# Kernel optimization log

Hardware: AMD Instinct MI355X
Metric: run time of the kernel (lower is better)

The kernel has to match this reference:

```python
import jax, jax.numpy as jnp
import numpy as np

B, SEQ, ST, DIN, DK, DV = 2, 4096, 128, 1024, 64, 64
T = SEQ + 2 * ST  # 4352, divisible by 8 -> no pad branch in original


def _l2norm(t):
    # matches torch F.normalize(p=2, dim=-1, eps=1e-12)
    return t / jnp.maximum(jnp.linalg.norm(t, axis=-1, keepdims=True), 1e-12)


def setup_inputs() -> dict:
    key = jax.random.key(0)
    ks = jax.random.split(key, 9)
    x = jax.random.normal(ks[0], (B, T, DIN), dtype=jnp.float32)
    w = 0.02
    Wq = jax.random.normal(ks[1], (DK, DIN), dtype=jnp.float32) * w
    Wk = jax.random.normal(ks[2], (DK, DIN), dtype=jnp.float32) * w
    Wv = jax.random.normal(ks[3], (DV, DIN), dtype=jnp.float32) * w
    Wq_s = jax.random.normal(ks[4], (DK, DIN), dtype=jnp.float32) * w
    Wk_s = jax.random.normal(ks[5], (DK, DIN), dtype=jnp.float32) * w
    Wv_s = jax.random.normal(ks[6], (DV, DIN), dtype=jnp.float32) * w
    cope_emb = jax.random.normal(ks[7], (DK, T), dtype=jnp.float32)  # (1, dim_key, seq_len+2*state_len) squeezed
    scale = jnp.array([0.125], dtype=jnp.float32)  # learnable scaling_factor param
    return {"x": x, "Wq": Wq, "Wk": Wk, "Wv": Wv, "Wq_s": Wq_s,
            "Wk_s": Wk_s, "Wv_s": Wv_s, "cope_emb": cope_emb, "scale": scale}


def reference(x, Wq, Wk, Wv, Wq_s, Wk_s, Wv_s, cope_emb, scale):
    # extract_state: start-state, sequence, end-state
    xs, xm, xe = x[:, :ST], x[:, ST:ST + SEQ], x[:, ST + SEQ:]
    # project (Linear, no bias) then L2-normalize each token vector
    q = jnp.concatenate([_l2norm(xs @ Wq_s.T), _l2norm(xm @ Wq.T), _l2norm(xe @ Wq_s.T)], axis=1)
    k = jnp.concatenate([_l2norm(xs @ Wk_s.T), _l2norm(xm @ Wk.T), _l2norm(xe @ Wk_s.T)], axis=1)
    v = jnp.concatenate([_l2norm(xs @ Wv_s.T), _l2norm(xm @ Wv.T), _l2norm(xe @ Wv_s.T)], axis=1)

    # q@k^T is used both for CoPE gates and (scaled) attention scores
    logits = jnp.einsum('btd,bsd->bts', q, k)  # (B, T, T)

    # --- CoPE bias ---
    gates = jax.nn.sigmoid(logits)
    pos = jnp.cumsum(gates[:, :, ::-1], axis=-1)[:, :, ::-1]  # flip-cumsum-flip
    pos = jnp.minimum(pos, jnp.float32(T - 1))
    pos_floor = jnp.floor(pos)
    pos_ceil = jnp.ceil(pos)
    w = pos - pos_floor
    logits_int = jnp.einsum('btd,dl->btl', q, cope_emb)  # (B, T, T)
    lc = jnp.take_along_axis(logits_int, pos_ceil.astype(jnp.int32), axis=-1)
    lf = jnp.take_along_axis(logits_int, pos_floor.astype(jnp.int32), axis=-1)
    cope_bias = lc * w + lf * (1.0 - w)

    # --- causal + state-token mask: tril, with end-state rows blocked from start-state cols ---
    i = jnp.arange(T)
    mask = i[:, None] >= i[None, :]
    blocked = (i[:, None] >= SEQ + ST) & (i[None, :] < ST)
    mask = mask & (~blocked)
    attn_bias = jnp.where(mask, 0.0, -jnp.inf)[None, :, :]

    scores = logits * scale[0] + attn_bias + cope_bias
    att = jax.nn.softmax(scores, axis=-1) @ v  # (B, T, DV)
    return att
```

## Files before the change

kernel.cpp:

```cpp
#include <hip/hip_runtime.h>
#include <math.h>

#define B_ 2
#define SEQ_ 4096
#define ST_ 128
#define T_ 4352
#define DIN_ 1024
#define NW 16
#define LMAX 3328
#define LPAD 3336
#define NSLICE 272
#define NROW 8704

typedef _Float16 f16;
typedef __attribute__((ext_vector_type(8))) _Float16 f16x8;
typedef __attribute__((ext_vector_type(4))) float f32x4;

#define OB_WH  0
#define OB_WL  786432
#define OB_QH  1572864
#define OB_QL  2686976
#define OB_KH  3801088
#define OB_KL  4915200
#define OB_VT  6029312
#define OB_CPT 7143424
#define OB_SS  7569408
#define OB_XH  17039360
#define OB_XL  34865152
#define NEED_NEW 52690944ull

#define WT4_OFF 0
#define Q_OFF   393216
#define KT_OFF  950272
#define V_OFF   1507328

__device__ __forceinline__ int wuid() {
  return __builtin_amdgcn_readfirstlane((int)(threadIdx.x >> 6));
}

template<int CTRL, int RM>
__device__ __forceinline__ float dppadd(float x) {
  int y = __builtin_amdgcn_update_dpp(0, __float_as_int(x), CTRL, RM, 0xf, true);
  return x + __int_as_float(y);
}
__device__ __forceinline__ float wave_iscan(float x) {
  x = dppadd<0x111, 0xf>(x);
  x = dppadd<0x112, 0xf>(x);
  x = dppadd<0x114, 0xf>(x);
  x = dppadd<0x118, 0xf>(x);
  x = dppadd<0x142, 0xa>(x);
  x = dppadd<0x143, 0xc>(x);
  return x;
}
__device__ __forceinline__ float p16scan(float x) {
  x = dppadd<0x111, 0xf>(x);
  x = dppadd<0x112, 0xf>(x);
  x = dppadd<0x114, 0xf>(x);
  x = dppadd<0x118, 0xf>(x);
  return x;
}
__device__ __forceinline__ float swz15(float x) {
  return __int_as_float(__builtin_amdgcn_ds_swizzle(__float_as_int(x), 0x1F0));
}

__global__ __launch_bounds__(256) void wsplit_kernel(
    const float* __restrict__ Wq,  const float* __restrict__ Wk,
    const float* __restrict__ Wv,  const float* __restrict__ Wqs,
    const float* __restrict__ Wks, const float* __restrict__ Wvs,
    f16* __restrict__ wh, f16* __restrict__ wl) {
  const int m = blockIdx.y;
  const float* src = (m==0)?Wq:(m==1)?Wqs:(m==2)?Wk:(m==3)?Wks:(m==4)?Wv:Wvs;
  const int g0 = (int)blockIdx.x * 4096 + (int)threadIdx.x * 16;
  const float4* s4 = reinterpret_cast<const float4*>(src + g0);
  float4 v0 = s4[0], v1 = s4[1], v2 = s4[2], v3 = s4[3];
  f16x8 h0, h1, l0, l1;
  h0[0]=(f16)v0.x; h0[1]=(f16)v0.y; h0[2]=(f16)v0.z; h0[3]=(f16)v0.w;
  h0[4]=(f16)v1.x; h0[5]=(f16)v1.y; h0[6]=(f16)v1.z; h0[7]=(f16)v1.w;
  h1[0]=(f16)v2.x; h1[1]=(f16)v2.y; h1[2]=(f16)v2.z; h1[3]=(f16)v2.w;
  h1[4]=(f16)v3.x; h1[5]=(f16)v3.y; h1[6]=(f16)v3.z; h1[7]=(f16)v3.w;
  l0[0]=(f16)(v0.x-(float)h0[0]); l0[1]=(f16)(v0.y-(float)h0[1]);
  l0[2]=(f16)(v0.z-(float)h0[2]); l0[3]=(f16)(v0.w-(float)h0[3]);
  l0[4]=(f16)(v1.x-(float)h0[4]); l0[5]=(f16)(v1.y-(float)h0[5]);
  l0[6]=(f16)(v1.z-(float)h0[6]); l0[7]=(f16)(v1.w-(float)h0[7]);
  l1[0]=(f16)(v2.x-(float)h1[0]); l1[1]=(f16)(v2.y-(float)h1[1]);
  l1[2]=(f16)(v2.z-(float)h1[2]); l1[3]=(f16)(v2.w-(float)h1[3]);
  l1[4]=(f16)(v3.x-(float)h1[4]); l1[5]=(f16)(v3.y-(float)h1[5]);
  l1[6]=(f16)(v3.z-(float)h1[6]); l1[7]=(f16)(v3.w-(float)h1[7]);
  const size_t o = (size_t)m * 65536 + g0;
  *reinterpret_cast<f16x8*>(wh + o) = h0;
  *reinterpret_cast<f16x8*>(wh + o + 8) = h1;
  *reinterpret_cast<f16x8*>(wl + o) = l0;
  *reinterpret_cast<f16x8*>(wl + o + 8) = l1;
}

__global__ __launch_bounds__(256) void xsplit_kernel(
    const float* __restrict__ x, f16* __restrict__ xh, f16* __restrict__ xl) {
  const size_t g0 = ((size_t)blockIdx.x * 256 + threadIdx.x) * 16;
  const float4* s4 = reinterpret_cast<const float4*>(x + g0);
  float4 v0 = s4[0], v1 = s4[1], v2 = s4[2], v3 = s4[3];
  f16x8 h0, h1, l0, l1;
  h0[0]=(f16)v0.x; h0[1]=(f16)v0.y; h0[2]=(f16)v0.z; h0[3]=(f16)v0.w;
  h0[4]=(f16)v1.x; h0[5]=(f16)v1.y; h0[6]=(f16)v1.z; h0[7]=(f16)v1.w;
  h1[0]=(f16)v2.x; h1[1]=(f16)v2.y; h1[2]=(f16)v2.z; h1[3]=(f16)v2.w;
  h1[4]=(f16)v3.x; h1[5]=(f16)v3.y; h1[6]=(f16)v3.z; h1[7]=(f16)v3.w;
  l0[0]=(f16)(v0.x-(float)h0[0]); l0[1]=(f16)(v0.y-(float)h0[1]);
  l0[2]=(f16)(v0.z-(float)h0[2]); l0[3]=(f16)(v0.w-(float)h0[3]);
  l0[4]=(f16)(v1.x-(float)h0[4]); l0[5]=(f16)(v1.y-(float)h0[5]);
  l0[6]=(f16)(v1.z-(float)h0[6]); l0[7]=(f16)(v1.w-(float)h0[7]);
  l1[0]=(f16)(v2.x-(float)h1[0]); l1[1]=(f16)(v2.y-(float)h1[1]);
  l1[2]=(f16)(v2.z-(float)h1[2]); l1[3]=(f16)(v2.w-(float)h1[3]);
  l1[4]=(f16)(v3.x-(float)h1[4]); l1[5]=(f16)(v3.y-(float)h1[5]);
  l1[6]=(f16)(v3.z-(float)h1[6]); l1[7]=(f16)(v3.w-(float)h1[7]);
  *reinterpret_cast<f16x8*>(xh + g0) = h0;
  *reinterpret_cast<f16x8*>(xh + g0 + 8) = h1;
  *reinterpret_cast<f16x8*>(xl + g0) = l0;
  *reinterpret_cast<f16x8*>(xl + g0 + 8) = l1;
}

__global__ __launch_bounds__(256) void copet_kernel(
    const float* __restrict__ cope, f16* __restrict__ copeT) {
  __shared__ float t2[64][65];
  const int l0 = blockIdx.x << 6;
  const int tid = (int)threadIdx.x;
  #pragma unroll
  for (int p = 0; p < 16; ++p) {
    int d = (p << 2) + (tid >> 6), c = tid & 63;
    t2[d][c] = cope[(size_t)d * T_ + l0 + c];
  }
  __syncthreads();
  #pragma unroll
  for (int p = 0; p < 16; ++p) {
    int l = (p << 2) + (tid >> 6), d = tid & 63;
    copeT[(size_t)(l0 + l) * 64 + d] = (f16)t2[d][l];
  }
}

#define PM_MFMA(ACC, WHP, WLP) { \
  f16x8 bh_ = *reinterpret_cast<const f16x8*>((WHP) + (st << 5)); \
  f16x8 bl_ = *reinterpret_cast<const f16x8*>((WLP) + (st << 5)); \
  ACC = __builtin_amdgcn_mfma_f32_16x16x32_f16(xh_, bh_, ACC, 0, 0, 0); \
  ACC = __builtin_amdgcn_mfma_f32_16x16x32_f16(xl_, bh_, ACC, 0, 0, 0); \
  ACC = __builtin_amdgcn_mfma_f32_16x16x32_f16(xh_, bl_, ACC, 0, 0, 0); }

#define PM_RED(ACC, P) { \
  float s0_ = ACC[0]*ACC[0], s1_ = ACC[1]*ACC[1], s2_ = ACC[2]*ACC[2], s3_ = ACC[3]*ACC[3]; \
  s0_ += __shfl_xor(s0_, 1, 64); s1_ += __shfl_xor(s1_, 1, 64); \
  s2_ += __shfl_xor(s2_, 1, 64); s3_ += __shfl_xor(s3_, 1, 64); \
  s0_ += __shfl_xor(s0_, 2, 64); s1_ += __shfl_xor(s1_, 2, 64); \
  s2_ += __shfl_xor(s2_, 2, 64); s3_ += __shfl_xor(s3_, 2, 64); \
  s0_ += __shfl_xor(s0_, 4, 64); s1_ += __shfl_xor(s1_, 4, 64); \
  s2_ += __shfl_xor(s2_, 4, 64); s3_ += __shfl_xor(s3_, 4, 64); \
  s0_ += __shfl_xor(s0_, 8, 64); s1_ += __shfl_xor(s1_, 8, 64); \
  s2_ += __shfl_xor(s2_, 8, 64); s3_ += __shfl_xor(s3_, 8, 64); \
  if (qlo == 0) { \
    ssq[wn][P][(qhi << 2) + 0] = s0_; ssq[wn][P][(qhi << 2) + 1] = s1_; \
    ssq[wn][P][(qhi << 2) + 2] = s2_; ssq[wn][P][(qhi << 2) + 3] = s3_; } }

#define PM_QK1(ACC, P, HH, LL, RG) { \
  float tt_ = ssq[0][P][(qhi << 2) + RG] + ssq[1][P][(qhi << 2) + RG] \
            + ssq[2][P][(qhi << 2) + RG] + ssq[3][P][(qhi << 2) + RG]; \
  float rn_ = 1.f / fmaxf(sqrtf(tt_), 1e-12f); \
  float v_ = ACC[RG] * rn_; \
  f16 h_ = (f16)v_; \
  size_t ad_ = (size_t)(bt0 + (qhi << 2) + RG) * 64 + (wn << 4) + qlo; \
  HH[ad_] = h_; LL[ad_] = (f16)(v_ - (float)h_); }

#define PM_V1(ACC, P, RG) { \
  float tt_ = ssq[0][P][(qhi << 2) + RG] + ssq[1][P][(qhi << 2) + RG] \
            + ssq[2][P][(qhi << 2) + RG] + ssq[3][P][(qhi << 2) + RG]; \
  float rn_ = 1.f / fmaxf(sqrtf(tt_), 1e-12f); \
  vt[(size_t)(b * 64 + (wn << 4) + qlo) * T_ + t0 + (qhi << 2) + RG] = (f16)(ACC[RG] * rn_); }

__global__ __launch_bounds__(512, 4) void projM_kernel(
    const f16* __restrict__ xh, const f16* __restrict__ xl,
    const f16* __restrict__ wh, const f16* __restrict__ wl,
    f16* __restrict__ qh, f16* __restrict__ ql,
    f16* __restrict__ kh, f16* __restrict__ kl,
    f16* __restrict__ vt) {
  __shared__ float ssq[4][3][16];
  __shared__ float part[4][64][12];
  const int lane = (int)threadIdx.x & 63;
  const int w = wuid();
  const int wn = w & 3;
  const int kh2 = w >> 2;
  const int qlo = lane & 15, qhi = lane >> 4;
  const int bt0 = (int)blockIdx.x << 4;
  const int b = bt0 / T_;
  const int t0 = bt0 - b * T_;
  const int spec = (t0 < ST_ || t0 >= ST_ + SEQ_) ? 1 : 0;

  const int kof = kh2 << 9;
  const f16* xhr = xh + (size_t)(bt0 + qlo) * DIN_ + kof + (qhi << 3);
  const f16* xlr = xl + (size_t)(bt0 + qlo) * DIN_ + kof + (qhi << 3);
  const size_t wrow = (size_t)((wn << 4) + qlo) * 1024 + kof + (qhi << 3);
  const f16* wq  = wh + (size_t)(0 + spec) * 65536 + wrow;
  const f16* wqL = wl + (size_t)(0 + spec) * 65536 + wrow;
  const f16* wk  = wh + (size_t)(2 + spec) * 65536 + wrow;
  const f16* wkL = wl + (size_t)(2 + spec) * 65536 + wrow;
  const f16* wv  = wh + (size_t)(4 + spec) * 65536 + wrow;
  const f16* wvL = wl + (size_t)(4 + spec) * 65536 + wrow;

  f32x4 aq = {0.f,0.f,0.f,0.f}, ak = {0.f,0.f,0.f,0.f}, av = {0.f,0.f,0.f,0.f};

  #pragma unroll 4
  for (int st = 0; st < 16; ++st) {
    f16x8 xh_ = *reinterpret_cast<const f16x8*>(xhr + (st << 5));
    f16x8 xl_ = *reinterpret_cast<const f16x8*>(xlr + (st << 5));
    PM_MFMA(aq, wq, wqL)
    PM_MFMA(ak, wk, wkL)
    PM_MFMA(av, wv, wvL)
  }

  if (w >= 4) {
    float* p = &part[w - 4][lane][0];
    p[0] = aq[0]; p[1] = aq[1]; p[2]  = aq[2]; p[3]  = aq[3];
    p[4] = ak[0]; p[5] = ak[1]; p[6]  = ak[2]; p[7]  = ak[3];
    p[8] = av[0]; p[9] = av[1]; p[10] = av[2]; p[11] = av[3];
  }
  __syncthreads();
  if (w < 4) {
    const float* p = &part[w][lane][0];
    aq[0] += p[0]; aq[1] += p[1]; aq[2] += p[2];  aq[3] += p[3];
    ak[0] += p[4]; ak[1] += p[5]; ak[2] += p[6];  ak[3] += p[7];
    av[0] += p[8]; av[1] += p[9]; av[2] += p[10]; av[3] += p[11];
    PM_RED(aq, 0) PM_RED(ak, 1) PM_RED(av, 2)
  }
  __syncthreads();
  if (w < 4) {
    PM_QK1(aq, 0, qh, ql, 0) PM_QK1(aq, 0, qh, ql, 1)
    PM_QK1(aq, 0, qh, ql, 2) PM_QK1(aq, 0, qh, ql, 3)
    PM_QK1(ak, 1, kh, kl, 0) PM_QK1(ak, 1, kh, kl, 1)
    PM_QK1(ak, 1, kh, kl, 2) PM_QK1(ak, 1, kh, kl, 3)
    PM_V1(av, 2, 0) PM_V1(av, 2, 1) PM_V1(av, 2, 2) PM_V1(av, 2, 3)
  }
}

__global__ __launch_bounds__(256) void gsum_kernel(
    const f16* __restrict__ qh, const f16* __restrict__ kh,
    float* __restrict__ ss) {
  const int lane = (int)threadIdx.x & 63;
  const int w = wuid();
  const int qlo = lane & 15, qhi = lane >> 4;
  const int chunk = blockIdx.x;
  const int bt0 = (int)blockIdx.y << 4;
  const int b = blockIdx.z;
  const int rowg0 = b * T_ + bt0;
  const size_t bT64 = (size_t)(b * T_) * 64;
  const f16* qrp = qh + (size_t)(rowg0 + qlo) * 64 + (qhi << 3);
  f16x8 aqh0 = *reinterpret_cast<const f16x8*>(qrp);
  f16x8 aqh1 = *reinterpret_cast<const f16x8*>(qrp + 32);
  #pragma unroll
  for (int nf = 0; nf < 8; ++nf) {
    const int colbase = (chunk << 9) + (w << 7) + (nf << 4);
    if (colbase < T_) {
      const int sg = colbase + qlo;
      const f16* krh_ = kh + bT64 + (size_t)sg * 64 + (qhi << 3);
      f16x8 bh0 = *reinterpret_cast<const f16x8*>(krh_);
      f16x8 bh1 = *reinterpret_cast<const f16x8*>(krh_ + 32);
      f32x4 a = {0.f, 0.f, 0.f, 0.f};
      a = __builtin_amdgcn_mfma_f32_16x16x32_f16(aqh0, bh0, a, 0, 0, 0);
      a = __builtin_amdgcn_mfma_f32_16x16x32_f16(aqh1, bh1, a, 0, 0, 0);
      float g0 = 1.f / (1.f + __expf(-a[0])); float s0 = p16scan(g0);
      float g1 = 1.f / (1.f + __expf(-a[1])); float s1 = p16scan(g1);
      float g2 = 1.f / (1.f + __expf(-a[2])); float s2 = p16scan(g2);
      float g3 = 1.f / (1.f + __expf(-a[3])); float s3 = p16scan(g3);
      if (qlo == 15) {
        const int sl = colbase >> 4;
        ss[(size_t)(rowg0 + (qhi << 2) + 0) * NSLICE + sl] = s0;
        ss[(size_t)(rowg0 + (qhi << 2) + 1) * NSLICE + sl] = s1;
        ss[(size_t)(rowg0 + (qhi << 2) + 2) * NSLICE + sl] = s2;
        ss[(size_t)(rowg0 + (qhi << 2) + 3) * NSLICE + sl] = s3;
      }
    }
  }
}

__global__ __launch_bounds__(1024) void sscan2_kernel(float* __restrict__ ss) {
  const int lane = (int)threadIdx.x & 63;
  const int w = wuid();
  const int row = (int)blockIdx.x * 16 + w;
  float* r = ss + (size_t)row * NSLICE;
  const int base = NSLICE - 1 - 5 * lane;
  double v0 = 0.0, v1 = 0.0, v2 = 0.0, v3 = 0.0, v4 = 0.0;
  double acc = 0.0;
  if (base - 0 >= 0) { acc += (double)r[base - 0]; } v0 = acc;
  if (base - 1 >= 0) { acc += (double)r[base - 1]; } v1 = acc;
  if (base - 2 >= 0) { acc += (double)r[base - 2]; } v2 = acc;
  if (base - 3 >= 0) { acc += (double)r[base - 3]; } v3 = acc;
  if (base - 4 >= 0) { acc += (double)r[base - 4]; } v4 = acc;
  double x = acc;
  #pragma unroll
  for (int off = 1; off < 64; off <<= 1) {
    double y = __shfl_up(x, off, 64);
    if (lane >= off) x += y;
  }
  const double offn = x - acc;
  if (base - 0 >= 0) r[base - 0] = (float)(v0 + offn);
  if (base - 1 >= 0) r[base - 1] = (float)(v1 + offn);
  if (base - 2 >= 0) r[base - 2] = (float)(v2 + offn);
  if (base - 3 >= 0) r[base - 3] = (float)(v3 + offn);
  if (base - 4 >= 0) r[base - 4] = (float)(v4 + offn);
}

#define QKD(SF, NF) { \
  int sg_ = swb + (NF << 4) + qlo; \
  int scl_ = sg_ < T_ ? sg_ : T_ - 1; \
  const f16* krh_ = kh + bT64 + (size_t)scl_ * 64 + (qhi << 3); \
  f16x8 bh0_ = *reinterpret_cast<const f16x8*>(krh_); \
  f16x8 bh1_ = *reinterpret_cast<const f16x8*>(krh_ + 32); \
  f32x4 a_ = {0.f, 0.f, 0.f, 0.f}; \
  a_ = __builtin_amdgcn_mfma_f32_16x16x32_f16(aqh0, bh0_, a_, 0, 0, 0); \
  a_ = __builtin_amdgcn_mfma_f32_16x16x32_f16(aqh1, bh1_, a_, 0, 0, 0); \
  SF = a_; }

#define PXA(SF, RG, SSV, LF, LC, WF) { \
  float g_ = 1.f / (1.f + __expf(-SF[RG])); \
  float in_ = p16scan(g_); \
  float pos_ = SSV - in_ + g_; \
  pos_ = pos_ < 0.f ? 0.f : (pos_ > 3326.f ? 3326.f : pos_); \
  int idx_ = (int)pos_; \
  WF = pos_ - (float)idx_; \
  const f16* lrow_ = liL + ((qhi << 2) + RG) * LPAD + idx_; \
  LF = (float)lrow_[0]; LC = (float)lrow_[1]; }

#define PXB(SF, NF, RG, LF, LC, WF) { \
  int sg_ = swb + (NF << 4) + qlo; \
  float bias_ = fmaf(WF, LC - LF, LF); \
  int tl_ = t0 + (qhi << 2) + RG; \
  bool valid_ = (sg_ <= tl_) && !((tl_ >= ST_ + SEQ_) && (sg_ < ST_)); \
  float p_ = valid_ ? __expf(fmaf(SF[RG], sc, bias_) - mrw[RG]) : 0.f; \
  lsum[RG] += p_; \
  pst[((qhi << 2) + RG) * 40 + (NF << 4) + qlo] = (f16)p_; }

#define PVF(OA, NF) { \
  int d_ = (NF << 4) + qlo; \
  const f16* vr_ = vt + (size_t)(b * 64 + d_) * T_; \
  f16x8 v0_ = *reinterpret_cast<const f16x8*>(vr_ + sv0); \
  OA = __builtin_amdgcn_mfma_f32_16x16x32_f16(pa0, v0_, OA, 0, 0, 0); }

#define OST(OA, NF) { \
  ob[w * 1024 + ((qhi << 2) + 0) * 64 + (NF << 4) + qlo] = OA[0]; \
  ob[w * 1024 + ((qhi << 2) + 1) * 64 + (NF << 4) + qlo] = OA[1]; \
  ob[w * 1024 + ((qhi << 2) + 2) * 64 + (NF << 4) + qlo] = OA[2]; \
  ob[w * 1024 + ((qhi << 2) + 3) * 64 + (NF << 4) + qlo] = OA[3]; }

__global__ __launch_bounds__(1024, 4) void attnD_kernel(
    const f16* __restrict__ qh, const f16* __restrict__ kh,
    const f16* __restrict__ vt, const f16* __restrict__ cpt,
    const float* __restrict__ ss,
    const float* __restrict__ scalep, float* __restrict__ out) {
  __shared__ __align__(16) f16 liL[16 * LPAD];
  __shared__ __align__(16) f16 pstage[NW * 16 * 40];
  __shared__ float totF[NW][16];
  __shared__ float rmxS[NW][16];

  const int tid = (int)threadIdx.x;
  const int lane = tid & 63;
  const int w = wuid();
  const int bt0 = ((int)(gridDim.x - 1 - blockIdx.x)) << 4;
  const int b = bt0 / T_;
  const int t0 = bt0 - b * T_;
  const float sc = scalep[0];
  const int qlo = lane & 15, qhi = lane >> 4;

  const f16* qrp = qh + (size_t)(bt0 + qlo) * 64 + (qhi << 3);
  f16x8 aqh0 = *reinterpret_cast<const f16x8*>(qrp);
  f16x8 aqh1 = *reinterpret_cast<const f16x8*>(qrp + 32);

  {
    f32x4 rm = {-1e30f, -1e30f, -1e30f, -1e30f};
    #pragma unroll 2
    for (int c = 0; c < 13; ++c) {
      const int lf = w * 208 + (c << 4);
      const f16* cr = cpt + (size_t)(lf + qlo) * 64 + (qhi << 3);
      f16x8 b0 = *reinterpret_cast<const f16x8*>(cr);
      f16x8 b1 = *reinterpret_cast<const f16x8*>(cr + 32);
      f32x4 a = {0.f, 0.f, 0.f, 0.f};
      a = __builtin_amdgcn_mfma_f32_16x16x32_f16(aqh0, b0, a, 0, 0, 0);
      a = __builtin_amdgcn_mfma_f32_16x16x32_f16(aqh1, b1, a, 0, 0, 0);
      f16 h0_ = (f16)a[0]; liL[((qhi << 2) + 0) * LPAD + lf + qlo] = h0_; rm[0] = fmaxf(rm[0], (float)h0_);
      f16 h1_ = (f16)a[1]; liL[((qhi << 2) + 1) * LPAD + lf + qlo] = h1_; rm[1] = fmaxf(rm[1], (float)h1_);
      f16 h2_ = (f16)a[2]; liL[((qhi << 2) + 2) * LPAD + lf + qlo] = h2_; rm[2] = fmaxf(rm[2], (float)h2_);
      f16 h3_ = (f16)a[3]; liL[((qhi << 2) + 3) * LPAD + lf + qlo] = h3_; rm[3] = fmaxf(rm[3], (float)h3_);
    }
    #pragma unroll
    for (int k = 1; k < 16; k <<= 1) {
      rm[0] = fmaxf(rm[0], __shfl_xor(rm[0], k, 64));
      rm[1] = fmaxf(rm[1], __shfl_xor(rm[1], k, 64));
      rm[2] = fmaxf(rm[2], __shfl_xor(rm[2], k, 64));
      rm[3] = fmaxf(rm[3], __shfl_xor(rm[3], k, 64));
    }
    if (qlo == 0) {
      rmxS[w][(qhi << 2) + 0] = rm[0];
      rmxS[w][(qhi << 2) + 1] = rm[1];
      rmxS[w][(qhi << 2) + 2] = rm[2];
      rmxS[w][(qhi << 2) + 3] = rm[3];
    }
  }
  __syncthreads();
  f32x4 mrw;
  #pragma unroll
  for (int reg = 0; reg < 4; ++reg) {
    float mm = rmxS[0][(qhi << 2) + reg];
    #pragma unroll
    for (int w2 = 1; w2 < NW; ++w2) mm = fmaxf(mm, rmxS[w2][(qhi << 2) + reg]);
    mrw[reg] = mm + fabsf(sc) + 2e-3f;
  }

  f16* pst = pstage + w * 640;
  const size_t bT64 = (size_t)(b * T_) * 64;
  const float* ssl = ss + (size_t)(bt0 + (qhi << 2)) * NSLICE;

  f32x4 o0 = {0.f,0.f,0.f,0.f}, o1 = {0.f,0.f,0.f,0.f};
  f32x4 o2 = {0.f,0.f,0.f,0.f}, o3 = {0.f,0.f,0.f,0.f};
  f32x4 lsum = {0.f,0.f,0.f,0.f};

  const int jtmax = (t0 + 15) >> 9;
  for (int jt = jtmax; jt >= 0; --jt) {
    const int swb = (jt << 9) + (w << 5);
    f32x4 sf0, sf1;
    QKD(sf0, 0) QKD(sf1, 1)
    const int sbr = swb >> 4;
    const int sb0 = sbr < (NSLICE - 1) ? sbr : (NSLICE - 1);
    const int sb1 = (sbr + 1) < (NSLICE - 1) ? (sbr + 1) : (NSLICE - 1);
    float sA0 = ssl[0 * NSLICE + sb0];
    float sA1 = ssl[1 * NSLICE + sb0];
    float sA2 = ssl[2 * NSLICE + sb0];
    float sA3 = ssl[3 * NSLICE + sb0];
    float sB0 = ssl[0 * NSLICE + sb1];
    float sB1 = ssl[1 * NSLICE + sb1];
    float sB2 = ssl[2 * NSLICE + sb1];
    float sB3 = ssl[3 * NSLICE + sb1];
    float lf0, lc0, wf0, lf1, lc1, wf1, lf2, lc2, wf2, lf3, lc3, wf3;
    float lf4, lc4, wf4, lf5, lc5, wf5, lf6, lc6, wf6, lf7, lc7, wf7;
    PXA(sf0, 0, sA0, lf0, lc0, wf0) PXA(sf0, 1, sA1, lf1, lc1, wf1)
    PXA(sf0, 2, sA2, lf2, lc2, wf2) PXA(sf0, 3, sA3, lf3, lc3, wf3)
    PXA(sf1, 0, sB0, lf4, lc4, wf4) PXA(sf1, 1, sB1, lf5, lc5, wf5)
    PXA(sf1, 2, sB2, lf6, lc6, wf6) PXA(sf1, 3, sB3, lf7, lc7, wf7)
    PXB(sf0, 0, 0, lf0, lc0, wf0) PXB(sf0, 0, 1, lf1, lc1, wf1)
    PXB(sf0, 0, 2, lf2, lc2, wf2) PXB(sf0, 0, 3, lf3, lc3, wf3)
    PXB(sf1, 1, 0, lf4, lc4, wf4) PXB(sf1, 1, 1, lf5, lc5, wf5)
    PXB(sf1, 1, 2, lf6, lc6, wf6) PXB(sf1, 1, 3, lf7, lc7, wf7)
    {
      const f16* pr = pst + qlo * 40;
      f16x8 pa0 = *reinterpret_cast<const f16x8*>(pr + (qhi << 3));
      int sv0 = swb + (qhi << 3);
      sv0 = sv0 < T_ - 8 ? sv0 : T_ - 8;
      PVF(o0, 0) PVF(o1, 1) PVF(o2, 2) PVF(o3, 3)
    }
  }

  #pragma unroll
  for (int k = 1; k < 16; k <<= 1) {
    lsum[0] += __shfl_xor(lsum[0], k, 64);
    lsum[1] += __shfl_xor(lsum[1], k, 64);
    lsum[2] += __shfl_xor(lsum[2], k, 64);
    lsum[3] += __shfl_xor(lsum[3], k, 64);
  }
  __syncthreads();
  if (qlo == 0) {
    totF[w][(qhi << 2) + 0] = lsum[0];
    totF[w][(qhi << 2) + 1] = lsum[1];
    totF[w][(qhi << 2) + 2] = lsum[2];
    totF[w][(qhi << 2) + 3] = lsum[3];
  }
  float* ob = reinterpret_cast<float*>(liL);
  OST(o0, 0) OST(o1, 1) OST(o2, 2) OST(o3, 3)
  __syncthreads();
  {
    const int r = tid >> 6, d = tid & 63;
    float L = 0.f, o = 0.f;
    #pragma unroll
    for (int w2 = 0; w2 < NW; ++w2) {
      L += totF[w2][r];
      o += ob[w2 * 1024 + tid];
    }
    out[(size_t)(bt0 + r) * 64 + d] = o / L;
  }
}

__global__ __launch_bounds__(256) void wtrans_kernel(
    const float* __restrict__ Wq,  const float* __restrict__ Wk,
    const float* __restrict__ Wv,  const float* __restrict__ Wqs,
    const float* __restrict__ Wks, const float* __restrict__ Wvs,
    float* __restrict__ ws) {
  const int m = blockIdx.y;
  const float* src = (m==0)?Wq:(m==1)?Wqs:(m==2)?Wk:(m==3)?Wks:(m==4)?Wv:Wvs;
  float* dst = ws + (size_t)m * (DIN_*64);
  const int bx = blockIdx.x;
  #pragma unroll
  for (int p = 0; p < 16; ++p) {
    int e = (int)threadIdx.x + (p << 8);
    int c = e & 3, o = (e >> 2) & 63;
    int i = (bx << 6) + (p << 2) + c;
    dst[(((bx << 4) + p) * 64 + o) * 4 + c] = src[o * DIN_ + i];
  }
}

__global__ __launch_bounds__(256) void proj_kernel(
    const float* __restrict__ x, float* __restrict__ ws) {
  __shared__ float tile[32][65];
  const int t0 = blockIdx.x << 5;
  const int b  = blockIdx.y;
  const int pj = blockIdx.z;
  const int spec = (t0 < ST_ || t0 >= ST_ + SEQ_) ? 1 : 0;
  const float4* W4 = reinterpret_cast<const float4*>(ws + WT4_OFF + (size_t)(pj*2 + spec) * (DIN_*64));
  const int lane = (int)threadIdx.x & 63;
  const int w = wuid();
  const float* xb = x + ((size_t)(b * T_ + t0 + (w << 3))) * DIN_;
  float acc[8] = {0.f,0.f,0.f,0.f,0.f,0.f,0.f,0.f};
  #pragma unroll 4
  for (int i4 = 0; i4 < 256; ++i4) {
    float4 wv = W4[(i4 << 6) + lane];
    #pragma unroll
    for (int r = 0; r < 8; ++r) {
      float4 xv = reinterpret_cast<const float4*>(xb + r * DIN_)[i4];
      acc[r] = fmaf(wv.x, xv.x, fmaf(wv.y, xv.y, fmaf(wv.z, xv.z, fmaf(wv.w, xv.w, acc[r]))));
    }
  }
  float outv[8];
  #pragma unroll
  for (int r = 0; r < 8; ++r) {
    float sq = acc[r] * acc[r];
    #pragma unroll
    for (int off = 32; off; off >>= 1) sq += __shfl_xor(sq, off, 64);
    float n = fmaxf(sqrtf(sq), 1e-12f);
    outv[r] = acc[r] / n;
  }
  const int trow = t0 + (w << 3);
  if (pj != 1) {
    float* dst = ws + (pj == 0 ? Q_OFF : V_OFF) + ((size_t)(b * T_ + trow)) * 64;
    #pragma unroll
    for (int r = 0; r < 8; ++r) dst[r * 64 + lane] = outv[r];
  } else {
    #pragma unroll
    for (int r = 0; r < 8; ++r) tile[(w << 3) + r][lane] = outv[r];
    __syncthreads();
    float* kt = ws + KT_OFF + (size_t)b * 16 * T_ * 4;
    #pragma unroll
    for (int p = 0; p < 8; ++p) {
      int e = (int)threadIdx.x + (p << 8);
      int c = e & 3, tt = (e >> 2) & 31, d4 = e >> 7;
      kt[((size_t)d4 * T_ + t0 + tt) * 4 + c] = tile[tt][(d4 << 2) + c];
    }
  }
}

__global__ __launch_bounds__(1024) void attn_kernel(
    const float* __restrict__ ws_c, const float* __restrict__ cope,
    const float* __restrict__ scalep, float* __restrict__ out) {
  __shared__ float li_s[8 * T_];
  __shared__ float pbuf[NW][8][32];
  __shared__ float totF[NW][8];
  __shared__ double suffD[NW][8];
  __shared__ double carryD[2][8];
  __shared__ float mlL[NW][8];
  __shared__ float wmax[NW][8];
  const int tid = (int)threadIdx.x;
  const int lane = tid & 63;
  const int w = wuid();
  const int t0 = ((int)(gridDim.x - 1 - blockIdx.x)) << 3;
  const int b  = blockIdx.y;
  const float* qrow = ws_c + Q_OFF + ((size_t)(b * T_ + t0)) * 64;
  const float* ktb  = ws_c + KT_OFF + (size_t)b * 16 * T_ * 4;
  const float* vb   = ws_c + V_OFF + ((size_t)b * T_) * 64;
  const float sc = scalep[0];
  if (tid < 8) carryD[0][tid] = 0.0;
  float lm[8];
  #pragma unroll
  for (int r = 0; r < 8; ++r) lm[r] = -INFINITY;
  for (int jt = 0; jt < 5; ++jt) {
    const int l = (jt << 10) + tid;
    if (l < T_) {
      float a[8] = {0,0,0,0,0,0,0,0};
      #pragma unroll 4
      for (int d4 = 0; d4 < 16; ++d4) {
        float c0 = cope[(d4 * 4 + 0) * T_ + l];
        float c1 = cope[(d4 * 4 + 1) * T_ + l];
        float c2 = cope[(d4 * 4 + 2) * T_ + l];
        float c3 = cope[(d4 * 4 + 3) * T_ + l];
        #pragma unroll
        for (int r = 0; r < 8; ++r) {
          float4 qq = *reinterpret_cast<const float4*>(qrow + r * 64 + (d4 << 2));
          a[r] = fmaf(c0, qq.x, fmaf(c1, qq.y, fmaf(c2, qq.z, fmaf(c3, qq.w, a[r]))));
        }
      }
      #pragma unroll
      for (int r = 0; r < 8; ++r) { li_s[r * T_ + l] = a[r]; lm[r] = fmaxf(lm[r], a[r]); }
    }
  }
  #pragma unroll
  for (int r = 0; r < 8; ++r) {
    #pragma unroll
    for (int off = 32; off; off >>= 1) lm[r] = fmaxf(lm[r], __shfl_xor(lm[r], off, 64));
  }
  if (lane == 0) {
    #pragma unroll
    for (int r = 0; r < 8; ++r) wmax[w][r] = lm[r];
  }
  __syncthreads();
  float mrow[8];
  #pragma unroll
  for (int r = 0; r < 8; ++r) {
    float mm = wmax[0][r];
    #pragma unroll
    for (int w2 = 1; w2 < NW; ++w2) mm = fmaxf(mm, wmax[w2][r]);
    mrow[r] = mm + fabsf(sc) + 1e-3f;
  }
  float acc[8]  = {0,0,0,0,0,0,0,0};
  float lsum[8] = {0,0,0,0,0,0,0,0};
  int par = 0;
  for (int jt = 4; jt >= 0; --jt) {
    const int s = (jt << 10) + tid;
    const bool sval = (s < T_);
    float lg[8] = {0,0,0,0,0,0,0,0};
    if (sval) {
      #pragma unroll 4
      for (int d4 = 0; d4 < 16; ++d4) {
        float4 kk = *reinterpret_cast<const float4*>(ktb + ((size_t)d4 * T_ + s) * 4);
        #pragma unroll
        for (int r = 0; r < 8; ++r) {
          float4 qq = *reinterpret_cast<const float4*>(qrow + r * 64 + (d4 << 2));
          lg[r] = fmaf(kk.x, qq.x, fmaf(kk.y, qq.y, fmaf(kk.z, qq.z, fmaf(kk.w, qq.w, lg[r]))));
        }
      }
    }
    float locsuf[8], gtot[8];
    #pragma unroll
    for (int r = 0; r < 8; ++r) {
      float g = sval ? 1.f / (1.f + __expf(-lg[r])) : 0.f;
      float xx = wave_iscan(g);
      float tt = __shfl(xx, 63, 64);
      locsuf[r] = tt - xx + g;
      gtot[r] = tt;
    }
    if (lane == 0) {
      #pragma unroll
      for (int r = 0; r < 8; ++r) totF[w][r] = gtot[r];
    }
    __syncthreads();
    if (tid < 128) {
      const int w2 = tid >> 3, r = tid & 7;
      float ssum = 0.f;
      for (int w3 = w2 + 1; w3 < NW; ++w3) ssum += totF[w3][r];
      suffD[w2][r] = carryD[par][r] + (double)ssum;
      if (w2 == 0) carryD[par ^ 1][r] = carryD[par][r] + (double)(ssum + totF[0][r]);
    }
    __syncthreads();
    par ^= 1;
    if ((jt << 10) > t0 + 7) continue;
    float p[8];
    #pragma unroll
    for (int r = 0; r < 8; ++r) {
      double posd = suffD[w][r] + (double)locsuf[r];
      if (posd > 4351.0) posd = 4351.0;
      int idx = (int)posd;
      float wf = (float)(posd - (double)idx);
      int idx2 = idx < 4351 ? idx + 1 : 4351;
      float lf = li_s[r * T_ + idx];
      float lc = li_s[r * T_ + idx2];
      float bias = fmaf(wf, lc - lf, lf);
      const int t = t0 + r;
      const bool valid = sval && (s <= t) && !((t >= ST_ + SEQ_) && (s < ST_));
      float score = valid ? fmaf(lg[r], sc, bias) : -INFINITY;
      p[r] = __expf(score - mrow[r]);
      lsum[r] += p[r];
    }
    const int sbase = (jt << 10) + (w << 6);
    if (sbase < T_) {
      #pragma unroll
      for (int pass = 0; pass < 2; ++pass) {
        if ((lane >> 5) == pass) {
          #pragma unroll
          for (int r = 0; r < 8; ++r) pbuf[w][r][lane & 31] = p[r];
        }
        const int s0 = sbase + (pass << 5);
        #pragma unroll 4
        for (int s4 = 0; s4 < 8; ++s4) {
          const int sb = s0 + (s4 << 2);
          float v0 = vb[(size_t)(sb + 0) * 64 + lane];
          float v1 = vb[(size_t)(sb + 1) * 64 + lane];
          float v2 = vb[(size_t)(sb + 2) * 64 + lane];
          float v3 = vb[(size_t)(sb + 3) * 64 + lane];
          #pragma unroll
          for (int r = 0; r < 8; ++r) {
            float4 pr = *reinterpret_cast<const float4*>(&pbuf[w][r][s4 << 2]);
            acc[r] = fmaf(pr.x, v0, fmaf(pr.y, v1, fmaf(pr.z, v2, fmaf(pr.w, v3, acc[r]))));
          }
        }
      }
    }
  }
  #pragma unroll
  for (int r = 0; r < 8; ++r) {
    #pragma unroll
    for (int off = 32; off; off >>= 1) lsum[r] += __shfl_xor(lsum[r], off, 64);
  }
  if (lane == 0) {
    #pragma unroll
    for (int r = 0; r < 8; ++r) mlL[w][r] = lsum[r];
  }
  float* pb = &pbuf[w][0][0];
  #pragma unroll
  for (int pass = 0; pass < 2; ++pass) {
    __syncthreads();
    #pragma unroll
    for (int rr = 0; rr < 4; ++rr) pb[rr * 64 + lane] = acc[pass * 4 + rr];
    __syncthreads();
    if (tid < 256) {
      const int rr = tid >> 6, d = tid & 63;
      const int r = pass * 4 + rr;
      float o = 0.f, L = 0.f;
      #pragma unroll
      for (int w2 = 0; w2 < NW; ++w2) {
        o += (&pbuf[w2][0][0])[rr * 64 + d];
        L += mlL[w2][r];
      }
      out[((size_t)(b * T_ + t0 + r)) * 64 + d] = o / L;
    }
  }
}

extern "C" void kernel_launch(void* const* d_in, const int* in_sizes, int n_in,
                              void* d_out, int out_size, void* d_ws, size_t ws_size,
                              hipStream_t stream) {
  const float* x    = (const float*)d_in[0];
  const float* Wq   = (const float*)d_in[1];
  const float* Wk   = (const float*)d_in[2];
  const float* Wv   = (const float*)d_in[3];
  const float* Wqs  = (const float*)d_in[4];
  const float* Wks  = (const float*)d_in[5];
  const float* Wvs  = (const float*)d_in[6];
  const float* cope = (const float*)d_in[7];
  const float* scl  = (const float*)d_in[8];
  float* outp = (float*)d_out;
  (void)in_sizes; (void)n_in; (void)out_size;

  if (ws_size >= NEED_NEW) {
    unsigned char* wb = (unsigned char*)d_ws;
    f16* whp = (f16*)(wb + OB_WH);
    f16* wlp = (f16*)(wb + OB_WL);
    f16* qh = (f16*)(wb + OB_QH);
    f16* ql = (f16*)(wb + OB_QL);
    f16* kh = (f16*)(wb + OB_KH);
    f16* kl = (f16*)(wb + OB_KL);
    f16* vt = (f16*)(wb + OB_VT);
    f16* cpt = (f16*)(wb + OB_CPT);
    float* ssp = (float*)(wb + OB_SS);
    f16* xhp = (f16*)(wb + OB_XH);
    f16* xlp = (f16*)(wb + OB_XL);
    hipLaunchKernelGGL(wsplit_kernel, dim3(16, 6), dim3(256), 0, stream,
                       Wq, Wk, Wv, Wqs, Wks, Wvs, whp, wlp);
    hipLaunchKernelGGL(xsplit_kernel, dim3(2176), dim3(256), 0, stream, x, xhp, xlp);
    hipLaunchKernelGGL(copet_kernel, dim3(52), dim3(256), 0, stream, cope, cpt);
    hipLaunchKernelGGL(projM_kernel, dim3(544), dim3(512), 0, stream,
                       xhp, xlp, whp, wlp, qh, ql, kh, kl, vt);
    hipLaunchKernelGGL(gsum_kernel, dim3(9, 272, 2), dim3(256), 0, stream,
                       qh, kh, ssp);
    hipLaunchKernelGGL(sscan2_kernel, dim3(544), dim3(1024), 0, stream, ssp);
    hipLaunchKernelGGL(attnD_kernel, dim3(544), dim3(1024), 0, stream,
                       qh, kh, vt, cpt, ssp, scl, outp);
  } else {
    float* ws = (float*)d_ws;
    hipLaunchKernelGGL(wtrans_kernel, dim3(16, 6), dim3(256), 0, stream,
                       Wq, Wk, Wv, Wqs, Wks, Wvs, ws);
    hipLaunchKernelGGL(proj_kernel, dim3(136, 2, 3), dim3(256), 0, stream, x, ws);
    hipLaunchKernelGGL(attn_kernel, dim3(544, 2), dim3(1024), 0, stream, ws, cope, scl, outp);
  }
}
```

Baseline: 255.3 us.

## Fuse gate slice-sum and suffix scan into one kernel; prefetch K tiles in attention

Merges the gate-sum kernel and the separate suffix-scan kernel into one gscan kernel. Each 512-thread block computes all 272 slice sums for 16 rows into shared memory, then scans them in place, so the intermediate buffer is no longer written and re-read through global memory and one launch goes away. The attention loop also software-prefetches the next iteration's K fragments and slice sums into registers before the current compute. This adds register pressure and gives fewer, larger blocks for the gate pass.

```diff
diff --git a/kernel.cpp b/kernel.cpp
--- a/kernel.cpp
+++ b/kernel.cpp
@@ -235,83 +235,87 @@
   }
 }
 
-__global__ __launch_bounds__(256) void gsum_kernel(
+__global__ __launch_bounds__(512, 4) void gscan_kernel(
     const f16* __restrict__ qh, const f16* __restrict__ kh,
     float* __restrict__ ss) {
+  __shared__ float sl[16][NSLICE];
   const int lane = (int)threadIdx.x & 63;
   const int w = wuid();
   const int qlo = lane & 15, qhi = lane >> 4;
-  const int chunk = blockIdx.x;
-  const int bt0 = (int)blockIdx.y << 4;
-  const int b = blockIdx.z;
-  const int rowg0 = b * T_ + bt0;
+  const int rowg0 = (int)blockIdx.x << 4;
+  const int b = rowg0 / T_;
   const size_t bT64 = (size_t)(b * T_) * 64;
   const f16* qrp = qh + (size_t)(rowg0 + qlo) * 64 + (qhi << 3);
   f16x8 aqh0 = *reinterpret_cast<const f16x8*>(qrp);
   f16x8 aqh1 = *reinterpret_cast<const f16x8*>(qrp + 32);
-  #pragma unroll
-  for (int nf = 0; nf < 8; ++nf) {
-    const int colbase = (chunk << 9) + (w << 7) + (nf << 4);
-    if (colbase < T_) {
-      const int sg = colbase + qlo;
-      const f16* krh_ = kh + bT64 + (size_t)sg * 64 + (qhi << 3);
-      f16x8 bh0 = *reinterpret_cast<const f16x8*>(krh_);
-      f16x8 bh1 = *reinterpret_cast<const f16x8*>(krh_ + 32);
-      f32x4 a = {0.f, 0.f, 0.f, 0.f};
-      a = __builtin_amdgcn_mfma_f32_16x16x32_f16(aqh0, bh0, a, 0, 0, 0);
-      a = __builtin_amdgcn_mfma_f32_16x16x32_f16(aqh1, bh1, a, 0, 0, 0);
-      float g0 = 1.f / (1.f + __expf(-a[0])); float s0 = p16scan(g0);
-      float g1 = 1.f / (1.f + __expf(-a[1])); float s1 = p16scan(g1);
-      float g2 = 1.f / (1.f + __expf(-a[2])); float s2 = p16scan(g2);
-      float g3 = 1.f / (1.f + __expf(-a[3])); float s3 = p16scan(g3);
-      if (qlo == 15) {
-        const int sl = colbase >> 4;
-        ss[(size_t)(rowg0 + (qhi << 2) + 0) * NSLICE + sl] = s0;
-        ss[(size_t)(rowg0 + (qhi << 2) + 1) * NSLICE + sl] = s1;
-        ss[(size_t)(rowg0 + (qhi << 2) + 2) * NSLICE + sl] = s2;
-        ss[(size_t)(rowg0 + (qhi << 2) + 3) * NSLICE + sl] = s3;
-      }
-    }
-  }
-}
-
-__global__ __launch_bounds__(1024) void sscan2_kernel(float* __restrict__ ss) {
-  const int lane = (int)threadIdx.x & 63;
-  const int w = wuid();
-  const int row = (int)blockIdx.x * 16 + w;
-  float* r = ss + (size_t)row * NSLICE;
-  const int base = NSLICE - 1 - 5 * lane;
-  double v0 = 0.0, v1 = 0.0, v2 = 0.0, v3 = 0.0, v4 = 0.0;
-  double acc = 0.0;
-  if (base - 0 >= 0) { acc += (double)r[base - 0]; } v0 = acc;
-  if (base - 1 >= 0) { acc += (double)r[base - 1]; } v1 = acc;
-  if (base - 2 >= 0) { acc += (double)r[base - 2]; } v2 = acc;
-  if (base - 3 >= 0) { acc += (double)r[base - 3]; } v3 = acc;
-  if (base - 4 >= 0) { acc += (double)r[base - 4]; } v4 = acc;
-  double x = acc;
-  #pragma unroll
-  for (int off = 1; off < 64; off <<= 1) {
-    double y = __shfl_up(x, off, 64);
-    if (lane >= off) x += y;
-  }
-  const double offn = x - acc;
-  if (base - 0 >= 0) r[base - 0] = (float)(v0 + offn);
-  if (base - 1 >= 0) r[base - 1] = (float)(v1 + offn);
-  if (base - 2 >= 0) r[base - 2] = (float)(v2 + offn);
-  if (base - 3 >= 0) r[base - 3] = (float)(v3 + offn);
-  if (base - 4 >= 0) r[base - 4] = (float)(v4 + offn);
-}
-
-#define QKD(SF, NF) { \
-  int sg_ = swb + (NF << 4) + qlo; \
-  int scl_ = sg_ < T_ ? sg_ : T_ - 1; \
-  const f16* krh_ = kh + bT64 + (size_t)scl_ * 64 + (qhi << 3); \
-  f16x8 bh0_ = *reinterpret_cast<const f16x8*>(krh_); \
-  f16x8 bh1_ = *reinterpret_cast<const f16x8*>(krh_ + 32); \
-  f32x4 a_ = {0.f, 0.f, 0.f, 0.f}; \
-  a_ = __builtin_amdgcn_mfma_f32_16x16x32_f16(aqh0, bh0_, a_, 0, 0, 0); \
-  a_ = __builtin_amdgcn_mfma_f32_16x16x32_f16(aqh1, bh1_, a_, 0, 0, 0); \
-  SF = a_; }
+
+  for (int i = 0; i < 34; ++i) {
+    const int sli = w * 34 + i;
+    const int sg = (sli << 4) + qlo;
+    const f16* krh_ = kh + bT64 + (size_t)sg * 64 + (qhi << 3);
+    f16x8 bh0 = *reinterpret_cast<const f16x8*>(krh_);
+    f16x8 bh1 = *reinterpret_cast<const f16x8*>(krh_ + 32);
+    f32x4 a = {0.f, 0.f, 0.f, 0.f};
+    a = __builtin_amdgcn_mfma_f32_16x16x32_f16(aqh0, bh0, a, 0, 0, 0);
+    a = __builtin_amdgcn_mfma_f32_16x16x32_f16(aqh1, bh1, a, 0, 0, 0);
+    float g0 = 1.f / (1.f + __expf(-a[0])); float s0 = p16scan(g0);
+    float g1 = 1.f / (1.f + __expf(-a[1])); float s1 = p16scan(g1);
+    float g2 = 1.f / (1.f + __expf(-a[2])); float s2 = p16scan(g2);
+    float g3 = 1.f / (1.f + __expf(-a[3])); float s3 = p16scan(g3);
+    if (qlo == 15) {
+      sl[(qhi << 2) + 0][sli] = s0;
+      sl[(qhi << 2) + 1][sli] = s1;
+      sl[(qhi << 2) + 2][sli] = s2;
+      sl[(qhi << 2) + 3][sli] = s3;
+    }
+  }
+  __syncthreads();
+  #pragma unroll
+  for (int rr = 0; rr < 2; ++rr) {
+    const int row = (w << 1) | rr;
+    const float* r = &sl[row][0];
+    const int base = NSLICE - 1 - 5 * lane;
+    double v0 = 0.0, v1 = 0.0, v2 = 0.0, v3 = 0.0, v4 = 0.0;
+    double acc = 0.0;
+    if (base - 0 >= 0) { acc += (double)r[base - 0]; } v0 = acc;
+    if (base - 1 >= 0) { acc += (double)r[base - 1]; } v1 = acc;
+    if (base - 2 >= 0) { acc += (double)r[base - 2]; } v2 = acc;
+    if (base - 3 >= 0) { acc += (double)r[base - 3]; } v3 = acc;
+    if (base - 4 >= 0) { acc += (double)r[base - 4]; } v4 = acc;
+    double x = acc;
+    #pragma unroll
+    for (int off = 1; off < 64; off <<= 1) {
+      double y = __shfl_up(x, off, 64);
+      if (lane >= off) x += y;
+    }
+    const double offn = x - acc;
+    float* go = ss + (size_t)(rowg0 + row) * NSLICE;
+    if (base - 0 >= 0) go[base - 0] = (float)(v0 + offn);
+    if (base - 1 >= 0) go[base - 1] = (float)(v1 + offn);
+    if (base - 2 >= 0) go[base - 2] = (float)(v2 + offn);
+    if (base - 3 >= 0) go[base - 3] = (float)(v3 + offn);
+    if (base - 4 >= 0) go[base - 4] = (float)(v4 + offn);
+  }
+}
+
+#define LDK2(SWB) { \
+  int sg0_ = (SWB) + qlo; int sc0_ = sg0_ < T_ ? sg0_ : T_ - 1; \
+  const f16* k0_ = kh + bT64 + (size_t)sc0_ * 64 + (qhi << 3); \
+  nk00 = *reinterpret_cast<const f16x8*>(k0_); \
+  nk01 = *reinterpret_cast<const f16x8*>(k0_ + 32); \
+  int sg1_ = (SWB) + 16 + qlo; int sc1_ = sg1_ < T_ ? sg1_ : T_ - 1; \
+  const f16* k1_ = kh + bT64 + (size_t)sc1_ * 64 + (qhi << 3); \
+  nk10 = *reinterpret_cast<const f16x8*>(k1_); \
+  nk11 = *reinterpret_cast<const f16x8*>(k1_ + 32); }
+
+#define LDSS(SWB) { \
+  int sbr_ = (SWB) >> 4; \
+  int sb0_ = sbr_ < (NSLICE - 1) ? sbr_ : (NSLICE - 1); \
+  int sb1_ = (sbr_ + 1) < (NSLICE - 1) ? (sbr_ + 1) : (NSLICE - 1); \
+  nsA0 = ssl[0 * NSLICE + sb0_]; nsA1 = ssl[1 * NSLICE + sb0_]; \
+  nsA2 = ssl[2 * NSLICE + sb0_]; nsA3 = ssl[3 * NSLICE + sb0_]; \
+  nsB0 = ssl[0 * NSLICE + sb1_]; nsB1 = ssl[1 * NSLICE + sb1_]; \
+  nsB2 = ssl[2 * NSLICE + sb1_]; nsB3 = ssl[3 * NSLICE + sb1_]; }
 
 #define PXA(SF, RG, SSV, LF, LC, WF) { \
   float g_ = 1.f / (1.f + __expf(-SF[RG])); \
@@ -415,22 +419,25 @@
   f32x4 o2 = {0.f,0.f,0.f,0.f}, o3 = {0.f,0.f,0.f,0.f};
   f32x4 lsum = {0.f,0.f,0.f,0.f};
 
+  f16x8 nk00, nk01, nk10, nk11;
+  float nsA0, nsA1, nsA2, nsA3, nsB0, nsB1, nsB2, nsB3;
   const int jtmax = (t0 + 15) >> 9;
+  {
+    const int swb0 = (jtmax << 9) + (w << 5);
+    LDK2(swb0) LDSS(swb0)
+  }
+
   for (int jt = jtmax; jt >= 0; --jt) {
     const int swb = (jt << 9) + (w << 5);
-    f32x4 sf0, sf1;
-    QKD(sf0, 0) QKD(sf1, 1)
-    const int sbr = swb >> 4;
-    const int sb0 = sbr < (NSLICE - 1) ? sbr : (NSLICE - 1);
-    const int sb1 = (sbr + 1) < (NSLICE - 1) ? (sbr + 1) : (NSLICE - 1);
-    float sA0 = ssl[0 * NSLICE + sb0];
-    float sA1 = ssl[1 * NSLICE + sb0];
-    float sA2 = ssl[2 * NSLICE + sb0];
-    float sA3 = ssl[3 * NSLICE + sb0];
-    float sB0 = ssl[0 * NSLICE + sb1];
-    float sB1 = ssl[1 * NSLICE + sb1];
-    float sB2 = ssl[2 * NSLICE + sb1];
-    float sB3 = ssl[3 * NSLICE + sb1];
+    f32x4 sf0 = {0.f, 0.f, 0.f, 0.f};
+    sf0 = __builtin_amdgcn_mfma_f32_16x16x32_f16(aqh0, nk00, sf0, 0, 0, 0);
+    sf0 = __builtin_amdgcn_mfma_f32_16x16x32_f16(aqh1, nk01, sf0, 0, 0, 0);
+    f32x4 sf1 = {0.f, 0.f, 0.f, 0.f};
+    sf1 = __builtin_amdgcn_mfma_f32_16x16x32_f16(aqh0, nk10, sf1, 0, 0, 0);
+    sf1 = __builtin_amdgcn_mfma_f32_16x16x32_f16(aqh1, nk11, sf1, 0, 0, 0);
+    float sA0 = nsA0, sA1 = nsA1, sA2 = nsA2, sA3 = nsA3;
+    float sB0 = nsB0, sB1 = nsB1, sB2 = nsB2, sB3 = nsB3;
+    if (jt > 0) { LDK2(swb - 512) LDSS(swb - 512) }
     float lf0, lc0, wf0, lf1, lc1, wf1, lf2, lc2, wf2, lf3, lc3, wf3;
     float lf4, lc4, wf4, lf5, lc5, wf5, lf6, lc6, wf6, lf7, lc7, wf7;
     PXA(sf0, 0, sA0, lf0, lc0, wf0) PXA(sf0, 1, sA1, lf1, lc1, wf1)
@@ -755,9 +762,7 @@
     hipLaunchKernelGGL(copet_kernel, dim3(52), dim3(256), 0, stream, cope, cpt);
     hipLaunchKernelGGL(projM_kernel, dim3(544), dim3(512), 0, stream,
                        xhp, xlp, whp, wlp, qh, ql, kh, kl, vt);
-    hipLaunchKernelGGL(gsum_kernel, dim3(9, 272, 2), dim3(256), 0, stream,
-                       qh, kh, ssp);
-    hipLaunchKernelGGL(sscan2_kernel, dim3(544), dim3(1024), 0, stream, ssp);
+    hipLaunchKernelGGL(gscan_kernel, dim3(544), dim3(512), 0, stream, qh, kh, ssp);
     hipLaunchKernelGGL(attnD_kernel, dim3(544), dim3(1024), 0, stream,
                        qh, kh, vt, cpt, ssp, scl, outp);
   } else {
```

Measured after the change: 262.1 us. 1.03x slower.

## Fuse gate slice-sum and suffix-scan kernels into one LDS-backed kernel

Applied to the files above, without the earlier changes.

Merges the gate-sum kernel and the separate suffix-scan kernel into one kernel. Each block handles 16 query rows across all key slices, keeps the per-slice partial sums in shared memory, then runs the double-precision reverse scan and writes the final prefix values. This removes one launch and the global write/read round trip of the partial-sum buffer. In exchange the grid shrinks from many small blocks to 544 blocks of 8 waves with a serial 34-iteration loop per wave, which lowers parallelism.

```diff
diff --git a/kernel.cpp b/kernel.cpp
--- a/kernel.cpp
+++ b/kernel.cpp
@@ -235,71 +235,67 @@
   }
 }
 
-__global__ __launch_bounds__(256) void gsum_kernel(
+__global__ __launch_bounds__(512, 4) void gscan_kernel(
     const f16* __restrict__ qh, const f16* __restrict__ kh,
     float* __restrict__ ss) {
+  __shared__ float sl[16][NSLICE];
   const int lane = (int)threadIdx.x & 63;
   const int w = wuid();
   const int qlo = lane & 15, qhi = lane >> 4;
-  const int chunk = blockIdx.x;
-  const int bt0 = (int)blockIdx.y << 4;
-  const int b = blockIdx.z;
-  const int rowg0 = b * T_ + bt0;
+  const int rowg0 = (int)blockIdx.x << 4;
+  const int b = rowg0 / T_;
   const size_t bT64 = (size_t)(b * T_) * 64;
   const f16* qrp = qh + (size_t)(rowg0 + qlo) * 64 + (qhi << 3);
   f16x8 aqh0 = *reinterpret_cast<const f16x8*>(qrp);
   f16x8 aqh1 = *reinterpret_cast<const f16x8*>(qrp + 32);
-  #pragma unroll
-  for (int nf = 0; nf < 8; ++nf) {
-    const int colbase = (chunk << 9) + (w << 7) + (nf << 4);
-    if (colbase < T_) {
-      const int sg = colbase + qlo;
-      const f16* krh_ = kh + bT64 + (size_t)sg * 64 + (qhi << 3);
-      f16x8 bh0 = *reinterpret_cast<const f16x8*>(krh_);
-      f16x8 bh1 = *reinterpret_cast<const f16x8*>(krh_ + 32);
-      f32x4 a = {0.f, 0.f, 0.f, 0.f};
-      a = __builtin_amdgcn_mfma_f32_16x16x32_f16(aqh0, bh0, a, 0, 0, 0);
-      a = __builtin_amdgcn_mfma_f32_16x16x32_f16(aqh1, bh1, a, 0, 0, 0);
-      float g0 = 1.f / (1.f + __expf(-a[0])); float s0 = p16scan(g0);
-      float g1 = 1.f / (1.f + __expf(-a[1])); float s1 = p16scan(g1);
-      float g2 = 1.f / (1.f + __expf(-a[2])); float s2 = p16scan(g2);
-      float g3 = 1.f / (1.f + __expf(-a[3])); float s3 = p16scan(g3);
-      if (qlo == 15) {
-        const int sl = colbase >> 4;
-        ss[(size_t)(rowg0 + (qhi << 2) + 0) * NSLICE + sl] = s0;
-        ss[(size_t)(rowg0 + (qhi << 2) + 1) * NSLICE + sl] = s1;
-        ss[(size_t)(rowg0 + (qhi << 2) + 2) * NSLICE + sl] = s2;
-        ss[(size_t)(rowg0 + (qhi << 2) + 3) * NSLICE + sl] = s3;
-      }
-    }
-  }
-}
-
-__global__ __launch_bounds__(1024) void sscan2_kernel(float* __restrict__ ss) {
-  const int lane = (int)threadIdx.x & 63;
-  const int w = wuid();
-  const int row = (int)blockIdx.x * 16 + w;
-  float* r = ss + (size_t)row * NSLICE;
-  const int base = NSLICE - 1 - 5 * lane;
-  double v0 = 0.0, v1 = 0.0, v2 = 0.0, v3 = 0.0, v4 = 0.0;
-  double acc = 0.0;
-  if (base - 0 >= 0) { acc += (double)r[base - 0]; } v0 = acc;
-  if (base - 1 >= 0) { acc += (double)r[base - 1]; } v1 = acc;
-  if (base - 2 >= 0) { acc += (double)r[base - 2]; } v2 = acc;
-  if (base - 3 >= 0) { acc += (double)r[base - 3]; } v3 = acc;
-  if (base - 4 >= 0) { acc += (double)r[base - 4]; } v4 = acc;
-  double x = acc;
-  #pragma unroll
-  for (int off = 1; off < 64; off <<= 1) {
-    double y = __shfl_up(x, off, 64);
-    if (lane >= off) x += y;
-  }
-  const double offn = x - acc;
-  if (base - 0 >= 0) r[base - 0] = (float)(v0 + offn);
-  if (base - 1 >= 0) r[base - 1] = (float)(v1 + offn);
-  if (base - 2 >= 0) r[base - 2] = (float)(v2 + offn);
-  if (base - 3 >= 0) r[base - 3] = (float)(v3 + offn);
-  if (base - 4 >= 0) r[base - 4] = (float)(v4 + offn);
+
+  for (int i = 0; i < 34; ++i) {
+    const int sli = w * 34 + i;
+    const int sg = (sli << 4) + qlo;
+    const f16* krh_ = kh + bT64 + (size_t)sg * 64 + (qhi << 3);
+    f16x8 bh0 = *reinterpret_cast<const f16x8*>(krh_);
+    f16x8 bh1 = *reinterpret_cast<const f16x8*>(krh_ + 32);
+    f32x4 a = {0.f, 0.f, 0.f, 0.f};
+    a = __builtin_amdgcn_mfma_f32_16x16x32_f16(aqh0, bh0, a, 0, 0, 0);
+    a = __builtin_amdgcn_mfma_f32_16x16x32_f16(aqh1, bh1, a, 0, 0, 0);
+    float g0 = 1.f / (1.f + __expf(-a[0])); float s0 = p16scan(g0);
+    float g1 = 1.f / (1.f + __expf(-a[1])); float s1 = p16scan(g1);
+    float g2 = 1.f / (1.f + __expf(-a[2])); float s2 = p16scan(g2);
+    float g3 = 1.f / (1.f + __expf(-a[3])); float s3 = p16scan(g3);
+    if (qlo == 15) {
+      sl[(qhi << 2) + 0][sli] = s0;
+      sl[(qhi << 2) + 1][sli] = s1;
+      sl[(qhi << 2) + 2][sli] = s2;
+      sl[(qhi << 2) + 3][sli] = s3;
+    }
+  }
+  __syncthreads();
+  #pragma unroll
+  for (int rr = 0; rr < 2; ++rr) {
+    const int row = (w << 1) | rr;
+    const float* r = &sl[row][0];
+    const int base = NSLICE - 1 - 5 * lane;
+    double v0 = 0.0, v1 = 0.0, v2 = 0.0, v3 = 0.0, v4 = 0.0;
+    double acc = 0.0;
+    if (base - 0 >= 0) { acc += (double)r[base - 0]; } v0 = acc;
+    if (base - 1 >= 0) { acc += (double)r[base - 1]; } v1 = acc;
+    if (base - 2 >= 0) { acc += (double)r[base - 2]; } v2 = acc;
+    if (base - 3 >= 0) { acc += (double)r[base - 3]; } v3 = acc;
+    if (base - 4 >= 0) { acc += (double)r[base - 4]; } v4 = acc;
+    double x = acc;
+    #pragma unroll
+    for (int off = 1; off < 64; off <<= 1) {
+      double y = __shfl_up(x, off, 64);
+      if (lane >= off) x += y;
+    }
+    const double offn = x - acc;
+    float* go = ss + (size_t)(rowg0 + row) * NSLICE;
+    if (base - 0 >= 0) go[base - 0] = (float)(v0 + offn);
+    if (base - 1 >= 0) go[base - 1] = (float)(v1 + offn);
+    if (base - 2 >= 0) go[base - 2] = (float)(v2 + offn);
+    if (base - 3 >= 0) go[base - 3] = (float)(v3 + offn);
+    if (base - 4 >= 0) go[base - 4] = (float)(v4 + offn);
+  }
 }
 
 #define QKD(SF, NF) { \
@@ -755,9 +751,7 @@
     hipLaunchKernelGGL(copet_kernel, dim3(52), dim3(256), 0, stream, cope, cpt);
     hipLaunchKernelGGL(projM_kernel, dim3(544), dim3(512), 0, stream,
                        xhp, xlp, whp, wlp, qh, ql, kh, kl, vt);
-    hipLaunchKernelGGL(gsum_kernel, dim3(9, 272, 2), dim3(256), 0, stream,
-                       qh, kh, ssp);
-    hipLaunchKernelGGL(sscan2_kernel, dim3(544), dim3(1024), 0, stream, ssp);
+    hipLaunchKernelGGL(gscan_kernel, dim3(544), dim3(512), 0, stream, qh, kh, ssp);
     hipLaunchKernelGGL(attnD_kernel, dim3(544), dim3(1024), 0, stream,
                        qh, kh, vt, cpt, ssp, scl, outp);
   } else {
```

Result: no change. 251.9 us (-1.3%).
